# Performance work log

Measured on AMD Instinct MI355X. Metric: run time of the kernel, lower is better.

## Reference

```python
import jax, jax.numpy as jnp
import numpy as np

DECAY = 0.99
EPS = 1e-5
K = 1024  # num_embeddings
D = 64    # embedding_dim


def setup_inputs() -> dict:
    key = jax.random.key(0)
    k1, k2 = jax.random.split(key)
    inputs = jax.random.normal(k1, (64, 64, 32, 32), dtype=jnp.float32)
    weight = jax.random.uniform(k2, (K, D), minval=-1.0 / K, maxval=1.0 / K, dtype=jnp.float32)
    cluster_size = jnp.zeros((K,), dtype=jnp.float32)
    embed_avg = weight.copy()
    return {"inputs": inputs, "weight": weight, "cluster_size": cluster_size, "embed_avg": embed_avg}


def reference(inputs, weight, cluster_size, embed_avg):
    B, _, H, W = inputs.shape
    # faithful to torch: raw memory-order view(-1, D), no channel permute
    flat = inputs.reshape(-1, D)  # (N, D), N = B*H*W
    distances = (jnp.sum(flat * flat, axis=1, keepdims=True)
                 + jnp.sum(weight * weight, axis=1)
                 - 2.0 * flat @ weight.T)
    idx = jnp.argmin(distances, axis=1)  # (N,)
    quantized = weight[idx].reshape(inputs.shape)  # == onehot @ weight, reshaped

    # EMA codebook update (training path)
    counts = jax.ops.segment_sum(jnp.ones(flat.shape[0], dtype=jnp.float32), idx, num_segments=K)
    cs = DECAY * cluster_size + (1.0 - DECAY) * counts
    n = jnp.sum(cs)
    cs = (cs + EPS) / (n + K * EPS) * n
    dw = jax.ops.segment_sum(flat, idx, num_segments=K)  # == onehot^T @ flat
    new_embed_avg = DECAY * embed_avg + (1.0 - DECAY) * dw
    new_weight = new_embed_avg / cs[:, None]

    # straight-through estimator
    quantized_st = inputs + jax.lax.stop_gradient(quantized - inputs)
    indices = idx.reshape(B, H, W)
    return quantized_st, indices, new_weight, cs, new_embed_avg
```

## Files before the change

kernel.cpp:

```cpp
#include <hip/hip_runtime.h>

#define NROWS 65536
#define KC    1024
#define DD    64

#define QOFF  0
#define IOFF  4194304
#define WOFF  4259840
#define CSOFF 4325376
#define EAOFF 4326400

#define WS_CODESQ  0
#define WS_COUNTS  1056
#define WS_RCCNT   2080
#define WS_CURSOR  2096
#define WS_OFFS    3120
#define WS_CSFIN   4144
#define WS_DW      5168
#define WS_WSWZ    70704
#define WS_IDX     137264
#define WS_RCLIST  202800
#define WS_ROWLIST 268336
#define WS_PACKED  333872

#define MARGIN 5e-5f

typedef _Float16 half8 __attribute__((ext_vector_type(8)));
typedef float    floatx4 __attribute__((ext_vector_type(4)));

struct F4 { float x, y, z, w; };
typedef const __attribute__((address_space(4))) F4    c4F4;
typedef const __attribute__((address_space(4))) float c4f;

__device__ __forceinline__ unsigned f2ord(float f) {
    unsigned u = __float_as_uint(f);
    return (u & 0x80000000u) ? ~u : (u | 0x80000000u);
}

__device__ __forceinline__ float rowsq4(const float4* xv) {
    float4 re, ro;
    re.x = __fmul_rn(xv[0].x, xv[0].x); re.y = __fmul_rn(xv[0].y, xv[0].y);
    re.z = __fmul_rn(xv[0].z, xv[0].z); re.w = __fmul_rn(xv[0].w, xv[0].w);
    ro.x = __fmul_rn(xv[1].x, xv[1].x); ro.y = __fmul_rn(xv[1].y, xv[1].y);
    ro.z = __fmul_rn(xv[1].z, xv[1].z); ro.w = __fmul_rn(xv[1].w, xv[1].w);
#pragma unroll
    for (int i = 2; i < 16; i += 2) {
        re.x = __fadd_rn(re.x, __fmul_rn(xv[i].x, xv[i].x));
        re.y = __fadd_rn(re.y, __fmul_rn(xv[i].y, xv[i].y));
        re.z = __fadd_rn(re.z, __fmul_rn(xv[i].z, xv[i].z));
        re.w = __fadd_rn(re.w, __fmul_rn(xv[i].w, xv[i].w));
        ro.x = __fadd_rn(ro.x, __fmul_rn(xv[i + 1].x, xv[i + 1].x));
        ro.y = __fadd_rn(ro.y, __fmul_rn(xv[i + 1].y, xv[i + 1].y));
        ro.z = __fadd_rn(ro.z, __fmul_rn(xv[i + 1].z, xv[i + 1].z));
        ro.w = __fadd_rn(ro.w, __fmul_rn(xv[i + 1].w, xv[i + 1].w));
    }
    return __fadd_rn(__fadd_rn(__fadd_rn(re.x, re.y), __fadd_rn(re.z, re.w)),
                     __fadd_rn(__fadd_rn(ro.x, ro.y), __fadd_rn(ro.z, ro.w)));
}

__global__ void prep_kernel(const float* __restrict__ weight,
                            float* __restrict__ code_sq,
                            _Float16* __restrict__ wswz,
                            float* __restrict__ counts,
                            int* __restrict__ rccnt) {
    int c = blockIdx.x * blockDim.x + threadIdx.x;
    if (c >= KC) return;
    counts[c] = 0.0f;
    if (c == 0) rccnt[0] = 0;
    float4 wv4[16];
    const float4* pw = reinterpret_cast<const float4*>(weight + (size_t)c * DD);
#pragma unroll
    for (int i = 0; i < 16; ++i) wv4[i] = pw[i];
    code_sq[c] = rowsq4(wv4);
    float w64[64];
#pragma unroll
    for (int i = 0; i < 16; ++i) {
        w64[4 * i] = wv4[i].x; w64[4 * i + 1] = wv4[i].y;
        w64[4 * i + 2] = wv4[i].z; w64[4 * i + 3] = wv4[i].w;
    }
    const int t32 = c >> 5;
    const int s16 = (c >> 4) & 1;
    const int cl  = c & 15;
    const size_t base = (size_t)t32 * 4096 + s16 * 2048 + cl * 8;
#pragma unroll
    for (int q = 0; q < 8; ++q) {
        half8 h, l;
#pragma unroll
        for (int j = 0; j < 8; ++j) {
            float s = w64[q * 8 + j] * 1024.0f;
            _Float16 hh = (_Float16)s;
            h[j] = hh;
            l[j] = (_Float16)(s - (float)hh);
        }
        *reinterpret_cast<half8*>(wswz + base + q * 128)        = h;
        *reinterpret_cast<half8*>(wswz + base + 1024 + q * 128) = l;
    }
}

__global__ __launch_bounds__(256, 4) void vq_scan(
    const float* __restrict__ x_in, const float* __restrict__ code_sq,
    const _Float16* __restrict__ wswz,
    float* __restrict__ out, float* __restrict__ counts,
    int* __restrict__ idxbuf, int* __restrict__ rccnt, int* __restrict__ rclist,
    unsigned long long* __restrict__ packed) {

    __shared__ __align__(16) _Float16 lds_b[2][4096];
    __shared__ float lds_csq[KC];
    __shared__ float sm1[4][32], sm2[4][32];
    __shared__ int   si1[4][32];

    const int tid  = threadIdx.x;
    const int lane = tid & 63;
    const int w    = tid >> 6;
    const int wm   = w & 1;
    const int wsel = w >> 1;
    const int l15  = lane & 15;
    const int g    = lane >> 4;

    const int blockRow0 = blockIdx.x * 64;
    const int waveRow0  = blockRow0 + wm * 32;

#pragma unroll
    for (int i = 0; i < 4; ++i) lds_csq[tid + i * 256] = code_sq[tid + i * 256];

    half8 ah[4], al[4];
#pragma unroll
    for (int t = 0; t < 2; ++t) {
#pragma unroll
        for (int kh = 0; kh < 2; ++kh) {
            const float4* p4 = reinterpret_cast<const float4*>(
                x_in + (size_t)(waveRow0 + t * 16 + l15) * DD + kh * 32 + g * 8);
            float4 v0 = p4[0], v1 = p4[1];
            float vals[8] = {v0.x, v0.y, v0.z, v0.w, v1.x, v1.y, v1.z, v1.w};
            half8 hh, ll;
#pragma unroll
            for (int j = 0; j < 8; ++j) {
                _Float16 h = (_Float16)vals[j];
                hh[j] = h;
                ll[j] = (_Float16)(vals[j] - (float)h);
            }
            ah[t * 2 + kh] = hh;
            al[t * 2 + kh] = ll;
        }
    }

    {
        const float4* s = reinterpret_cast<const float4*>(wswz);
        reinterpret_cast<float4*>(lds_b[0])[tid]       = s[tid];
        reinterpret_cast<float4*>(lds_b[0])[tid + 256] = s[tid + 256];
    }
    __syncthreads();

    float m1[2][4], m2[2][4];
    int   i1[2][4];
#pragma unroll
    for (int t = 0; t < 2; ++t)
#pragma unroll
        for (int r = 0; r < 4; ++r) { m1[t][r] = INFINITY; m2[t][r] = INFINITY; i1[t][r] = 0; }

    int cur = 0;
    for (int ct = 0; ct < 32; ++ct) {
        float4 r0, r1;
        if (ct < 31) {
            const float4* s = reinterpret_cast<const float4*>(wswz + (size_t)(ct + 1) * 4096);
            r0 = s[tid];
            r1 = s[tid + 256];
        }

        const _Float16* S = lds_b[cur] + wsel * 2048;
        half8 bh0 = *reinterpret_cast<const half8*>(S + g * 128 + l15 * 8);
        half8 bh1 = *reinterpret_cast<const half8*>(S + 512 + g * 128 + l15 * 8);
        half8 bl0 = *reinterpret_cast<const half8*>(S + 1024 + g * 128 + l15 * 8);
        half8 bl1 = *reinterpret_cast<const half8*>(S + 1536 + g * 128 + l15 * 8);
        const int code = ct * 32 + wsel * 16 + l15;
        const float csq = lds_csq[code];
#pragma unroll
        for (int t = 0; t < 2; ++t) {
            floatx4 c1 = {0.f, 0.f, 0.f, 0.f};
            floatx4 c2 = {0.f, 0.f, 0.f, 0.f};
            c1 = __builtin_amdgcn_mfma_f32_16x16x32_f16(al[t * 2 + 0], bh0, c1, 0, 0, 0);
            c2 = __builtin_amdgcn_mfma_f32_16x16x32_f16(al[t * 2 + 1], bh1, c2, 0, 0, 0);
            c1 = __builtin_amdgcn_mfma_f32_16x16x32_f16(ah[t * 2 + 0], bl0, c1, 0, 0, 0);
            c2 = __builtin_amdgcn_mfma_f32_16x16x32_f16(ah[t * 2 + 1], bl1, c2, 0, 0, 0);
            c1 = __builtin_amdgcn_mfma_f32_16x16x32_f16(ah[t * 2 + 0], bh0, c1, 0, 0, 0);
            c2 = __builtin_amdgcn_mfma_f32_16x16x32_f16(ah[t * 2 + 1], bh1, c2, 0, 0, 0);
#pragma unroll
            for (int r = 0; r < 4; ++r) {
                float s = fmaf(c1[r] + c2[r], -0x1p-9f, csq);
                float mo = m1[t][r];
                m2[t][r] = fminf(fmaxf(s, mo), m2[t][r]);
                i1[t][r] = (s < mo) ? code : i1[t][r];
                m1[t][r] = fminf(mo, s);
            }
        }

        if (ct < 31) {
            reinterpret_cast<float4*>(lds_b[cur ^ 1])[tid]       = r0;
            reinterpret_cast<float4*>(lds_b[cur ^ 1])[tid + 256] = r1;
        }
        __syncthreads();
        cur ^= 1;
    }

#pragma unroll
    for (int t = 0; t < 2; ++t)
#pragma unroll
        for (int r = 0; r < 4; ++r)
#pragma unroll
            for (int mk = 1; mk < 16; mk <<= 1) {
                float o1 = __shfl_xor(m1[t][r], mk);
                float o2 = __shfl_xor(m2[t][r], mk);
                int   oi = __shfl_xor(i1[t][r], mk);
                float n2 = fminf(fminf(m2[t][r], o2), fmaxf(m1[t][r], o1));
                bool sel = (o1 < m1[t][r]) || (o1 == m1[t][r] && oi < i1[t][r]);
                m1[t][r] = sel ? o1 : m1[t][r];
                i1[t][r] = sel ? oi : i1[t][r];
                m2[t][r] = n2;
            }

    if (l15 == 0) {
#pragma unroll
        for (int t = 0; t < 2; ++t)
#pragma unroll
            for (int r = 0; r < 4; ++r) {
                int rib = t * 16 + g * 4 + r;
                sm1[w][rib] = m1[t][r];
                sm2[w][rib] = m2[t][r];
                si1[w][rib] = i1[t][r];
            }
    }
    __syncthreads();

    if (tid < 64) {
        int pwm = tid >> 5;
        int rib = tid & 31;
        float bm1 = sm1[pwm][rib], bm2 = sm2[pwm][rib];
        int bi = si1[pwm][rib];
        {
            float v1 = sm1[pwm + 2][rib];
            float v2 = sm2[pwm + 2][rib];
            int   vi = si1[pwm + 2][rib];
            if (v1 < bm1 || (v1 == bm1 && vi < bi)) {
                bm2 = fminf(bm1, v2);
                bm1 = v1; bi = vi;
            } else {
                bm2 = fminf(bm2, v1);
            }
        }
        int grow = blockRow0 + pwm * 32 + rib;
        if (bm2 - bm1 >= MARGIN) {
            idxbuf[grow] = bi;
            out[IOFF + grow] = (float)bi;
            atomicAdd(&counts[bi], 1.0f);
        } else {
            packed[grow] = 0xFFFFFFFFFFFFFFFFull;
            int pos = atomicAdd(rccnt, 1);
            rclist[pos] = grow;
        }
    }
}

__global__ __launch_bounds__(256, 4) void vq_recheck(
    const float* __restrict__ x_in, const float* __restrict__ weight,
    const float* __restrict__ code_sq,
    unsigned long long* __restrict__ packed,
    const int* __restrict__ rccnt, const int* __restrict__ rclist) {

    const int nrc = rccnt[0];
    const int nitems = ((nrc + 63) >> 6) * 16;

    const int tid  = threadIdx.x;
    const int lane = tid & 63;
    const int wvu  = __builtin_amdgcn_readfirstlane(tid >> 6);

    for (int item = blockIdx.x; item < nitems; item += gridDim.x) {
        const int rb     = (item >> 4) * 64;
        const int cchunk = item & 15;
        const bool valid = (rb + lane) < nrc;
        const int  grow  = rclist[valid ? rb + lane : rb];

        float4 xv[16];
        const float4* px = reinterpret_cast<const float4*>(x_in + (size_t)grow * DD);
#pragma unroll
        for (int i = 0; i < 16; ++i) xv[i] = px[i];
        const float rs = rowsq4(xv);

        const int k0 = cchunk * 64 + wvu * 16;
        unsigned long long wa = (unsigned long long)(weight + (size_t)k0 * DD);
        unsigned long long ca = (unsigned long long)(code_sq + k0);
        unsigned wal = __builtin_amdgcn_readfirstlane((unsigned)wa);
        unsigned wah = __builtin_amdgcn_readfirstlane((unsigned)(wa >> 32));
        unsigned cal = __builtin_amdgcn_readfirstlane((unsigned)ca);
        unsigned cah = __builtin_amdgcn_readfirstlane((unsigned)(ca >> 32));
        c4F4* wb4 = (c4F4*)(((unsigned long long)wah << 32) | wal);
        c4f*  cb  = (c4f*)(((unsigned long long)cah << 32) | cal);

        float best = INFINITY;
        int bidx = 0x7fffffff;

#pragma unroll 2
        for (int k = 0; k < 16; ++k) {
            float a0 = 0.f, a1 = 0.f, a2 = 0.f, a3 = 0.f;
#pragma unroll
            for (int i = 0; i < 16; ++i) {
                F4 w4;
                w4.x = wb4[k * 16 + i].x;
                w4.y = wb4[k * 16 + i].y;
                w4.z = wb4[k * 16 + i].z;
                w4.w = wb4[k * 16 + i].w;
                a0 += xv[i].x * w4.x;
                a1 += xv[i].y * w4.y;
                a2 += xv[i].z * w4.z;
                a3 += xv[i].w * w4.w;
            }
            float dot = (a0 + a1) + (a2 + a3);
            float csq = cb[k];
            float dst = __fsub_rn(__fadd_rn(rs, csq), __fmul_rn(2.0f, dot));
            int kg = k0 + k;
            if (dst < best) { best = dst; bidx = kg; }
        }

        if (valid) {
            unsigned long long p =
                ((unsigned long long)f2ord(best) << 32) | (unsigned)bidx;
            atomicMin(&packed[grow], p);
        }
    }
}

__global__ void rc_offsets_cs(const unsigned long long* __restrict__ packed,
                              const int* __restrict__ rccnt,
                              const int* __restrict__ rclist,
                              const float* __restrict__ cluster_size,
                              float* __restrict__ out, int* __restrict__ idxbuf,
                              float* __restrict__ counts,
                              int* __restrict__ offs, int* __restrict__ cursor,
                              float* __restrict__ cs_fin) {
    __shared__ int   hist[1024];
    __shared__ int   sc[1024];
    __shared__ float sb[1024];
    int k = threadIdx.x;
    hist[k] = 0;
    __syncthreads();
    const int nrc = rccnt[0];
    for (int i = k; i < nrc; i += 1024) {
        int grow = rclist[i];
        int bidx = (int)(packed[grow] & 0xFFFFFFFFull);
        out[IOFF + grow] = (float)bidx;
        idxbuf[grow] = bidx;
        atomicAdd(&hist[bidx], 1);
    }
    __syncthreads();
    int c = (int)counts[k] + hist[k];
    counts[k] = (float)c;
    float ce = 0.99f * cluster_size[k] + 0.01f * (float)c;
    sc[k] = c;
    sb[k] = ce;
    __syncthreads();
    for (int off = 1; off < 1024; off <<= 1) {
        int v = (k >= off) ? sc[k - off] : 0;
        __syncthreads();
        sc[k] += v;
        __syncthreads();
    }
    offs[k] = sc[k] - c;
    cursor[k] = 0;
    for (int off = 512; off > 0; off >>= 1) {
        if (k < off) sb[k] += sb[k + off];
        __syncthreads();
    }
    float n = sb[0];
    float v = ((ce + 1e-5f) / (n + 0.01024f)) * n;
    out[CSOFF + k] = v;
    cs_fin[k] = v;
}

__global__ void scatter_kernel(const int* __restrict__ idxbuf,
                               const int* __restrict__ offs,
                               int* __restrict__ cursor,
                               int* __restrict__ rowlist) {
    int r = blockIdx.x * blockDim.x + threadIdx.x;
    if (r >= NROWS) return;
    int k = idxbuf[r];
    int pos = atomicAdd(&cursor[k], 1);
    rowlist[offs[k] + pos] = r;
}

__global__ void dw_q_kernel(const float* __restrict__ x_in,
                            const float* __restrict__ weight,
                            const float* __restrict__ counts,
                            const int* __restrict__ offs,
                            const int* __restrict__ rowlist,
                            const float* __restrict__ embed_avg,
                            const float* __restrict__ cs_fin,
                            float* __restrict__ out, float* __restrict__ dw) {
    __shared__ float wsh[64];
    __shared__ float part[4][64];

    const int k    = blockIdx.x;
    const int tid  = threadIdx.x;
    const int lane = tid & 63;
    const int wv   = tid >> 6;

    if (tid < 64) wsh[tid] = weight[(size_t)k * DD + tid];
    __syncthreads();

    const int cnt  = (int)counts[k];
    const int base = offs[k];
    const float wk = wsh[lane];

    float acc = 0.f;
    int i = wv;
    for (; i + 12 < cnt; i += 16) {
        int r0 = rowlist[base + i];
        int r1 = rowlist[base + i + 4];
        int r2 = rowlist[base + i + 8];
        int r3 = rowlist[base + i + 12];
        float x0 = x_in[(size_t)r0 * DD + lane];
        float x1 = x_in[(size_t)r1 * DD + lane];
        float x2 = x_in[(size_t)r2 * DD + lane];
        float x3 = x_in[(size_t)r3 * DD + lane];
        out[QOFF + (size_t)r0 * DD + lane] = __fadd_rn(x0, __fsub_rn(wk, x0));
        out[QOFF + (size_t)r1 * DD + lane] = __fadd_rn(x1, __fsub_rn(wk, x1));
        out[QOFF + (size_t)r2 * DD + lane] = __fadd_rn(x2, __fsub_rn(wk, x2));
        out[QOFF + (size_t)r3 * DD + lane] = __fadd_rn(x3, __fsub_rn(wk, x3));
        acc = __fadd_rn(acc, x0);
        acc = __fadd_rn(acc, x1);
        acc = __fadd_rn(acc, x2);
        acc = __fadd_rn(acc, x3);
    }
    for (; i < cnt; i += 4) {
        int r = rowlist[base + i];
        float xq = x_in[(size_t)r * DD + lane];
        out[QOFF + (size_t)r * DD + lane] = __fadd_rn(xq, __fsub_rn(wk, xq));
        acc = __fadd_rn(acc, xq);
    }
    part[wv][lane] = acc;
    __syncthreads();
    if (tid < 64) {
        float s = __fadd_rn(__fadd_rn(part[0][tid], part[1][tid]),
                            __fadd_rn(part[2][tid], part[3][tid]));
        int e = k * DD + tid;
        dw[e] = s;
        float na = 0.99f * embed_avg[e] + 0.01f * s;
        out[EAOFF + e] = na;
        out[WOFF + e] = na / cs_fin[k];
    }
}

extern "C" void kernel_launch(void* const* d_in, const int* in_sizes, int n_in,
                              void* d_out, int out_size, void* d_ws, size_t ws_size,
                              hipStream_t stream) {
    (void)in_sizes; (void)n_in; (void)out_size; (void)ws_size;
    const float* x       = (const float*)d_in[0];
    const float* weight  = (const float*)d_in[1];
    const float* cluster = (const float*)d_in[2];
    const float* eavg    = (const float*)d_in[3];
    float* out = (float*)d_out;
    float* wsf = (float*)d_ws;

    float*    code_sq = wsf + WS_CODESQ;
    float*    counts  = wsf + WS_COUNTS;
    int*      rccnt   = (int*)(wsf + WS_RCCNT);
    int*      cursor  = (int*)(wsf + WS_CURSOR);
    int*      offs    = (int*)(wsf + WS_OFFS);
    float*    cs_fin  = wsf + WS_CSFIN;
    float*    dwbuf   = wsf + WS_DW;
    _Float16* wswz    = (_Float16*)(wsf + WS_WSWZ);
    int*      idxbuf  = (int*)(wsf + WS_IDX);
    int*      rclist  = (int*)(wsf + WS_RCLIST);
    int*      rowlist = (int*)(wsf + WS_ROWLIST);
    unsigned long long* packed = (unsigned long long*)(wsf + WS_PACKED);

    hipLaunchKernelGGL(prep_kernel, dim3(16), dim3(64), 0, stream,
                       weight, code_sq, wswz, counts, rccnt);
    hipLaunchKernelGGL(vq_scan, dim3(1024), dim3(256), 0, stream,
                       x, code_sq, wswz, out, counts, idxbuf, rccnt, rclist,
                       packed);
    hipLaunchKernelGGL(vq_recheck, dim3(2048), dim3(256), 0, stream,
                       x, weight, code_sq, packed, rccnt, rclist);
    hipLaunchKernelGGL(rc_offsets_cs, dim3(1), dim3(1024), 0, stream,
                       packed, rccnt, rclist, cluster, out, idxbuf, counts,
                       offs, cursor, cs_fin);
    hipLaunchKernelGGL(scatter_kernel, dim3(256), dim3(256), 0, stream,
                       idxbuf, offs, cursor, rowlist);
    hipLaunchKernelGGL(dw_q_kernel, dim3(1024), dim3(256), 0, stream,
                       x, weight, counts, offs, rowlist, eavg, cs_fin, out, dwbuf);
}
```

Baseline: 120.9 us.

## Stream codebook tiles to LDS with direct global_load_lds and bigger stages

```diff
diff --git a/kernel.cpp b/kernel.cpp
--- a/kernel.cpp
+++ b/kernel.cpp
@@ -104,7 +104,7 @@
     int* __restrict__ idxbuf, int* __restrict__ rccnt, int* __restrict__ rclist,
     unsigned long long* __restrict__ packed) {
 
-    __shared__ __align__(16) _Float16 lds_b[2][4096];
+    __shared__ __align__(16) _Float16 lds_b[2][8192];
     __shared__ float lds_csq[KC];
     __shared__ float sm1[4][32], sm2[4][32];
     __shared__ int   si1[4][32];
@@ -120,6 +120,16 @@
     const int blockRow0 = blockIdx.x * 64;
     const int waveRow0  = blockRow0 + wm * 32;
 
+    char* gsrc0 = const_cast<char*>(reinterpret_cast<const char*>(wswz));
+
+#pragma unroll
+    for (int j = 0; j < 4; ++j) {
+        __builtin_amdgcn_global_load_lds(
+            (__attribute__((address_space(1))) void*)(gsrc0 + tid * 16 + j * 4096),
+            (__attribute__((address_space(3))) void*)((char*)lds_b[0] + tid * 16 + j * 4096),
+            16, 0, 0);
+    }
+
 #pragma unroll
     for (int i = 0; i < 4; ++i) lds_csq[tid + i * 256] = code_sq[tid + i * 256];
 
@@ -143,12 +153,6 @@
             al[t * 2 + kh] = ll;
         }
     }
-
-    {
-        const float4* s = reinterpret_cast<const float4*>(wswz);
-        reinterpret_cast<float4*>(lds_b[0])[tid]       = s[tid];
-        reinterpret_cast<float4*>(lds_b[0])[tid + 256] = s[tid + 256];
-    }
     __syncthreads();
 
     float m1[2][4], m2[2][4];
@@ -159,45 +163,49 @@
         for (int r = 0; r < 4; ++r) { m1[t][r] = INFINITY; m2[t][r] = INFINITY; i1[t][r] = 0; }
 
     int cur = 0;
-    for (int ct = 0; ct < 32; ++ct) {
-        float4 r0, r1;
-        if (ct < 31) {
-            const float4* s = reinterpret_cast<const float4*>(wswz + (size_t)(ct + 1) * 4096);
-            r0 = s[tid];
-            r1 = s[tid + 256];
-        }
-
-        const _Float16* S = lds_b[cur] + wsel * 2048;
-        half8 bh0 = *reinterpret_cast<const half8*>(S + g * 128 + l15 * 8);
-        half8 bh1 = *reinterpret_cast<const half8*>(S + 512 + g * 128 + l15 * 8);
-        half8 bl0 = *reinterpret_cast<const half8*>(S + 1024 + g * 128 + l15 * 8);
-        half8 bl1 = *reinterpret_cast<const half8*>(S + 1536 + g * 128 + l15 * 8);
-        const int code = ct * 32 + wsel * 16 + l15;
-        const float csq = lds_csq[code];
-#pragma unroll
-        for (int t = 0; t < 2; ++t) {
-            floatx4 c1 = {0.f, 0.f, 0.f, 0.f};
-            floatx4 c2 = {0.f, 0.f, 0.f, 0.f};
-            c1 = __builtin_amdgcn_mfma_f32_16x16x32_f16(al[t * 2 + 0], bh0, c1, 0, 0, 0);
-            c2 = __builtin_amdgcn_mfma_f32_16x16x32_f16(al[t * 2 + 1], bh1, c2, 0, 0, 0);
-            c1 = __builtin_amdgcn_mfma_f32_16x16x32_f16(ah[t * 2 + 0], bl0, c1, 0, 0, 0);
-            c2 = __builtin_amdgcn_mfma_f32_16x16x32_f16(ah[t * 2 + 1], bl1, c2, 0, 0, 0);
-            c1 = __builtin_amdgcn_mfma_f32_16x16x32_f16(ah[t * 2 + 0], bh0, c1, 0, 0, 0);
-            c2 = __builtin_amdgcn_mfma_f32_16x16x32_f16(ah[t * 2 + 1], bh1, c2, 0, 0, 0);
-#pragma unroll
-            for (int r = 0; r < 4; ++r) {
-                float s = fmaf(c1[r] + c2[r], -0x1p-9f, csq);
-                float mo = m1[t][r];
-                m2[t][r] = fminf(fmaxf(s, mo), m2[t][r]);
-                i1[t][r] = (s < mo) ? code : i1[t][r];
-                m1[t][r] = fminf(mo, s);
-            }
-        }
-
-        if (ct < 31) {
-            reinterpret_cast<float4*>(lds_b[cur ^ 1])[tid]       = r0;
-            reinterpret_cast<float4*>(lds_b[cur ^ 1])[tid + 256] = r1;
-        }
+    for (int p = 0; p < 16; ++p) {
+        if (p < 15) {
+            char* src = gsrc0 + (size_t)(p + 1) * 16384;
+            char* dst = (char*)lds_b[cur ^ 1];
+#pragma unroll
+            for (int j = 0; j < 4; ++j) {
+                __builtin_amdgcn_global_load_lds(
+                    (__attribute__((address_space(1))) void*)(src + tid * 16 + j * 4096),
+                    (__attribute__((address_space(3))) void*)(dst + tid * 16 + j * 4096),
+                    16, 0, 0);
+            }
+        }
+
+#pragma unroll
+        for (int half = 0; half < 2; ++half) {
+            const _Float16* S = lds_b[cur] + half * 4096 + wsel * 2048;
+            half8 bh0 = *reinterpret_cast<const half8*>(S + g * 128 + l15 * 8);
+            half8 bh1 = *reinterpret_cast<const half8*>(S + 512 + g * 128 + l15 * 8);
+            half8 bl0 = *reinterpret_cast<const half8*>(S + 1024 + g * 128 + l15 * 8);
+            half8 bl1 = *reinterpret_cast<const half8*>(S + 1536 + g * 128 + l15 * 8);
+            const int code = p * 64 + half * 32 + wsel * 16 + l15;
+            const float csq = lds_csq[code];
+#pragma unroll
+            for (int t = 0; t < 2; ++t) {
+                floatx4 c1 = {0.f, 0.f, 0.f, 0.f};
+                floatx4 c2 = {0.f, 0.f, 0.f, 0.f};
+                c1 = __builtin_amdgcn_mfma_f32_16x16x32_f16(al[t * 2 + 0], bh0, c1, 0, 0, 0);
+                c2 = __builtin_amdgcn_mfma_f32_16x16x32_f16(al[t * 2 + 1], bh1, c2, 0, 0, 0);
+                c1 = __builtin_amdgcn_mfma_f32_16x16x32_f16(ah[t * 2 + 0], bl0, c1, 0, 0, 0);
+                c2 = __builtin_amdgcn_mfma_f32_16x16x32_f16(ah[t * 2 + 1], bl1, c2, 0, 0, 0);
+                c1 = __builtin_amdgcn_mfma_f32_16x16x32_f16(ah[t * 2 + 0], bh0, c1, 0, 0, 0);
+                c2 = __builtin_amdgcn_mfma_f32_16x16x32_f16(ah[t * 2 + 1], bh1, c2, 0, 0, 0);
+#pragma unroll
+                for (int r = 0; r < 4; ++r) {
+                    float s = fmaf(c1[r] + c2[r], -0x1p-9f, csq);
+                    float mo = m1[t][r];
+                    m2[t][r] = fminf(fmaxf(s, mo), m2[t][r]);
+                    i1[t][r] = (s < mo) ? code : i1[t][r];
+                    m1[t][r] = fminf(mo, s);
+                }
+            }
+        }
+
         __syncthreads();
         cur ^= 1;
     }
```

Result: no change. 119.8 us (-1.0%).
